# Performance work log

Hardware: AMD Instinct MI355X
Metric: run time of the kernel (lower is better)

## Reference

```python
import jax, jax.numpy as jnp
import numpy as np

D_MODEL = 1024
H = 16
D_K = D_MODEL // H
D_FF = 4096
EPS = 1e-6


def setup_inputs() -> dict:
    key = jax.random.key(0)
    ks = jax.random.split(key, 16)
    s = 1.0 / np.sqrt(D_MODEL)
    sf = 1.0 / np.sqrt(D_FF)
    inp = {
        'x': jax.random.normal(ks[0], (4, 2048, D_MODEL), dtype=jnp.float32),
        'wq': jax.random.uniform(ks[1], (D_MODEL, D_MODEL), minval=-s, maxval=s),
        'bq': jax.random.uniform(ks[2], (D_MODEL,), minval=-s, maxval=s),
        'wk': jax.random.uniform(ks[3], (D_MODEL, D_MODEL), minval=-s, maxval=s),
        'bk': jax.random.uniform(ks[4], (D_MODEL,), minval=-s, maxval=s),
        'wv': jax.random.uniform(ks[5], (D_MODEL, D_MODEL), minval=-s, maxval=s),
        'bv': jax.random.uniform(ks[6], (D_MODEL,), minval=-s, maxval=s),
        'wo': jax.random.uniform(ks[7], (D_MODEL, D_MODEL), minval=-s, maxval=s),
        'bo': jax.random.uniform(ks[8], (D_MODEL,), minval=-s, maxval=s),
        'w1': jax.random.uniform(ks[9], (D_MODEL, D_FF), minval=-s, maxval=s),
        'b1': jax.random.uniform(ks[10], (D_FF,), minval=-s, maxval=s),
        'w2': jax.random.uniform(ks[11], (D_FF, D_MODEL), minval=-sf, maxval=sf),
        'b2': jax.random.uniform(ks[12], (D_MODEL,), minval=-sf, maxval=sf),
        'alpha1': jnp.ones((1,), jnp.float32),
        'bias1': jnp.zeros((1,), jnp.float32),
        'alpha2': jnp.ones((1,), jnp.float32),
        'bias2': jnp.zeros((1,), jnp.float32),
    }
    return inp


def _layer_norm(x, alpha, bias):
    # torch: alpha*(x-mean)/(std+eps)+bias with unbiased std (ddof=1), eps on std
    m = jnp.mean(x, axis=-1, keepdims=True)
    s = jnp.std(x, axis=-1, keepdims=True, ddof=1)
    return alpha * (x - m) / (s + EPS) + bias


def _mha(x, wq, bq, wk, bk, wv, bv, wo, bo):
    B, S, _ = x.shape
    q = (x @ wq + bq).reshape(B, S, H, D_K).transpose(0, 2, 1, 3)
    k = (x @ wk + bk).reshape(B, S, H, D_K).transpose(0, 2, 1, 3)
    v = (x @ wv + bv).reshape(B, S, H, D_K).transpose(0, 2, 1, 3)
    scores = jnp.einsum('bhqd,bhkd->bhqk', q, k) / np.sqrt(D_K)
    attn = jax.nn.softmax(scores, axis=-1)
    out = jnp.einsum('bhqk,bhkd->bhqd', attn, v)
    out = out.transpose(0, 2, 1, 3).reshape(B, S, D_MODEL)
    return out @ wo + bo


def reference(x, wq, bq, wk, bk, wv, bv, wo, bo, w1, b1, w2, b2,
              alpha1, bias1, alpha2, bias2):
    # Residual 1: x + MHA(LN(x))
    h = x + _mha(_layer_norm(x, alpha1, bias1), wq, bq, wk, bk, wv, bv, wo, bo)
    # Residual 2: h + FFN(LN(h)); FFN = W2 relu(W1 z + b1) + b2
    z = _layer_norm(h, alpha2, bias2)
    ffn = jax.nn.relu(z @ w1 + b1) @ w2 + b2
    return h + ffn
```

## Files before the change

### kernel.cpp

```cpp
#include <hip/hip_runtime.h>
#include <hip/hip_bf16.h>
#include <cstdint>
#include <cstddef>

typedef __bf16 bf16;
typedef __bf16 bf16x4 __attribute__((ext_vector_type(4)));
typedef __bf16 bf16x8 __attribute__((ext_vector_type(8)));
typedef float f32x4 __attribute__((ext_vector_type(4)));

#define QK_SCALE 0.1803368801111204f

#define AS1 __attribute__((address_space(1)))
#define AS3 __attribute__((address_space(3)))

__device__ __forceinline__ void gload_lds16(const void* g, void* l) {
  __builtin_amdgcn_global_load_lds((AS1 void*)g, (AS3 void*)l, 16, 0, 0);
}

__device__ __forceinline__ float b2f(unsigned short u) {
  union { unsigned int i; float f; } v; v.i = (unsigned int)u << 16; return v.f;
}

__global__ __launch_bounds__(256)
void transpose_cvt(const float* __restrict__ in, bf16* __restrict__ out,
                   int K, int N) {
  __shared__ float t[32][33];
  const int tx = threadIdx.x, ty = threadIdx.y;
  const int n0 = blockIdx.x * 32, k0 = blockIdx.y * 32;
#pragma unroll
  for (int j = ty; j < 32; j += 8)
    t[j][tx] = in[(size_t)(k0 + j) * N + n0 + tx];
  __syncthreads();
#pragma unroll
  for (int j = ty; j < 32; j += 8)
    out[(size_t)(n0 + j) * K + k0 + tx] = (bf16)t[tx][j];
}

__global__ __launch_bounds__(256)
void transpose_cvt4(const float* __restrict__ wq, const float* __restrict__ wk,
                    const float* __restrict__ wv, const float* __restrict__ wo,
                    bf16* __restrict__ wqkvT, bf16* __restrict__ woT) {
  __shared__ float t[32][33];
  const int tx = threadIdx.x, ty = threadIdx.y, z = blockIdx.z;
  const float* in = (z == 0) ? wq : (z == 1) ? wk : (z == 2) ? wv : wo;
  bf16* out = (z < 3) ? wqkvT + (size_t)z * 1024 * 1024 : woT;
  const float sc = (z == 0) ? QK_SCALE : 1.0f;
  const int n0 = blockIdx.x * 32, k0 = blockIdx.y * 32;
#pragma unroll
  for (int j = ty; j < 32; j += 8)
    t[j][tx] = in[(size_t)(k0 + j) * 1024 + n0 + tx] * sc;
  __syncthreads();
#pragma unroll
  for (int j = ty; j < 32; j += 8)
    out[(size_t)(n0 + j) * 1024 + k0 + tx] = (bf16)t[tx][j];
}

__global__ __launch_bounds__(256)
void concat_bias(const float* __restrict__ bq, const float* __restrict__ bk,
                 const float* __restrict__ bv, float* __restrict__ o) {
  int i = blockIdx.x * 256 + threadIdx.x;
  if (i < 1024) o[i] = bq[i] * QK_SCALE;
  else if (i < 2048) o[i] = bk[i - 1024];
  else o[i] = bv[i - 2048];
}

__global__ __launch_bounds__(256)
void ln_kernel(const float* __restrict__ x, bf16* __restrict__ y,
               const float* __restrict__ alpha_p, const float* __restrict__ beta_p) {
  const int row = blockIdx.x;
  const float4 v = ((const float4*)(x + (size_t)row * 1024))[threadIdx.x];
  float s = v.x + v.y + v.z + v.w;
  float ss = v.x * v.x + v.y * v.y + v.z * v.z + v.w * v.w;
#pragma unroll
  for (int m = 1; m < 64; m <<= 1) {
    s += __shfl_xor(s, m);
    ss += __shfl_xor(ss, m);
  }
  __shared__ float red[8];
  const int wave = threadIdx.x >> 6, lane = threadIdx.x & 63;
  if (lane == 0) { red[wave] = s; red[4 + wave] = ss; }
  __syncthreads();
  s = red[0] + red[1] + red[2] + red[3];
  ss = red[4] + red[5] + red[6] + red[7];
  const float mean = s * (1.0f / 1024.0f);
  const float var = fmaxf(ss - 1024.0f * mean * mean, 0.0f) * (1.0f / 1023.0f);
  const float k = alpha_p[0] / (sqrtf(var) + 1e-6f);
  const float beta = beta_p[0];
  union { bf16 b[4]; uint2 u; } pk;
  pk.b[0] = (bf16)((v.x - mean) * k + beta);
  pk.b[1] = (bf16)((v.y - mean) * k + beta);
  pk.b[2] = (bf16)((v.z - mean) * k + beta);
  pk.b[3] = (bf16)((v.w - mean) * k + beta);
  ((uint2*)(y + (size_t)row * 1024))[threadIdx.x] = pk.u;
}

template <typename OutT, bool RELU, bool RESID>
__global__ __launch_bounds__(256)
void gemm_bt(const bf16* __restrict__ A, const bf16* __restrict__ Bt,
             const float* __restrict__ bias, const float* __restrict__ resid,
             OutT* __restrict__ C, int M, int N, int K) {
  __shared__ __align__(16) bf16 As[2][128 * 32];
  __shared__ __align__(16) bf16 Bs[2][128 * 32];
  const int tid = threadIdx.x;
  const int wave = tid >> 6, lane = tid & 63;
  const int l16 = lane & 15, lq = lane >> 4;
  const int nwg = gridDim.x * gridDim.y;
  const int id = blockIdx.y * gridDim.x + blockIdx.x;
  const int w = (id & 7) * (nwg >> 3) + (id >> 3);
  const int bm = (w / gridDim.y) * 128, bn = (w % gridDim.y) * 128;
  const int wr = wave >> 1, wc = wave & 1;

  const int tmp = (lane * 16) ^ (((lane >> 3) & 7) << 4);
  const int srow = tmp >> 6, sseg = (tmp >> 4) & 3;
  const bf16* Ab = A + (size_t)bm * K + sseg * 8;
  const bf16* Bb = Bt + (size_t)bn * K + sseg * 8;

  auto STAGE = [&](int k0, int buf) {
#pragma unroll
    for (int i = 0; i < 2; i++) {
      const int chunk = wave * 2 + i;
      const int r = chunk * 16 + srow;
      gload_lds16(Ab + (size_t)r * K + k0, (char*)As[buf] + chunk * 1024);
      gload_lds16(Bb + (size_t)r * K + k0, (char*)Bs[buf] + chunk * 1024);
    }
  };
  auto swz = [&](int row) -> int {
    return (row >> 1) * 128 + (((((row & 1) << 2) | lq) ^ ((row >> 1) & 7)) << 4);
  };

  STAGE(0, 0);
  __syncthreads();

  f32x4 acc[4][4] = {};
  const int nk = K >> 5;
  for (int t = 0; t < nk; t++) {
    const int cur = t & 1;
    if (t + 1 < nk) STAGE((t + 1) << 5, cur ^ 1);
    bf16x8 a[4], b[4];
#pragma unroll
    for (int m = 0; m < 4; m++)
      a[m] = *(const bf16x8*)((const char*)As[cur] + swz(wr * 64 + m * 16 + l16));
#pragma unroll
    for (int n = 0; n < 4; n++)
      b[n] = *(const bf16x8*)((const char*)Bs[cur] + swz(wc * 64 + n * 16 + l16));
#pragma unroll
    for (int m = 0; m < 4; m++)
#pragma unroll
      for (int n = 0; n < 4; n++)
        acc[m][n] = __builtin_amdgcn_mfma_f32_16x16x32_bf16(a[m], b[n], acc[m][n], 0, 0, 0);
    __syncthreads();
  }
#pragma unroll
  for (int m = 0; m < 4; m++) {
    const int row0 = bm + wr * 64 + m * 16 + lq * 4;
#pragma unroll
    for (int n = 0; n < 4; n++) {
      const int col = bn + wc * 64 + n * 16 + l16;
      const float bv = bias[col];
#pragma unroll
      for (int j = 0; j < 4; j++) {
        float v = acc[m][n][j] + bv;
        if (RELU) v = fmaxf(v, 0.0f);
        if (RESID) v += resid[(size_t)(row0 + j) * N + col];
        C[(size_t)(row0 + j) * N + col] = (OutT)v;
      }
    }
  }
}

template <typename OutT, bool RELU, bool BIAS>
__global__ __launch_bounds__(512, 2)
void gemm_v4(const bf16* __restrict__ A, const bf16* __restrict__ Bt,
             const float* __restrict__ bias, OutT* __restrict__ C,
             int lda, int ldb, int ldc, int K,
             int azs, int bzs, size_t czs) {
  __shared__ __align__(16) char lds[4 * 32768];
  const int tid = threadIdx.x;
  const int wave = tid >> 6, lane = tid & 63;
  const int l16 = lane & 15, lq = lane >> 4;
  const int wr = wave >> 2, wc = wave & 3;
  const int nwg = gridDim.x * gridDim.y;
  const int id = blockIdx.y * gridDim.x + blockIdx.x;
  const int w = (id & 7) * (nwg >> 3) + (id >> 3);
  const int bm = (w / gridDim.y) * 256, bn = (w % gridDim.y) * 256;

  A  += (size_t)blockIdx.z * azs;
  Bt += (size_t)blockIdx.z * bzs;
  C  += (size_t)blockIdx.z * czs;

  const int p = lane >> 3, jj = (lane & 7) ^ p;
  const int lrow = p * 2 + (jj >> 2), lseg = jj & 3;
  const bf16* Abase = A + (size_t)bm * lda + lseg * 8;
  const bf16* Bbase = Bt + (size_t)bn * ldb + lseg * 8;

  auto STAGEH = [&](int t, int half) {
    const int k0 = t << 5;
    const int grow = (half & 1) * 128 + wave * 16 + lrow;
    const void* src = (half < 2) ? (const void*)(Abase + (size_t)grow * lda + k0)
                                 : (const void*)(Bbase + (size_t)grow * ldb + k0);
    gload_lds16(src, lds + (t & 3) * 32768 + (half >> 1) * 16384 +
                         (half & 1) * 8192 + wave * 1024);
  };
  auto swz = [&](int row) -> int {
    return (row >> 1) * 128 + (((((row & 1) << 2) | lq) ^ ((row >> 1) & 7)) << 4);
  };

  const int nkt = K >> 5;
#pragma unroll
  for (int hh = 0; hh < 4; hh++) STAGEH(0, hh);
#pragma unroll
  for (int hh = 0; hh < 4; hh++) STAGEH(1, hh);
  asm volatile("s_waitcnt vmcnt(4)" ::: "memory");
  __builtin_amdgcn_s_barrier();

  f32x4 acc[8][4] = {};
  for (int t = 0; t < nkt; t++) {
    const char* bufA = lds + (t & 3) * 32768;
    const char* bufB = bufA + 16384;
    bf16x8 a0[4], b0[4], a1[4];
#pragma unroll
    for (int i = 0; i < 4; i++)
      a0[i] = *(const bf16x8*)(bufA + swz(wr * 128 + i * 16 + l16));
#pragma unroll
    for (int n = 0; n < 4; n++)
      b0[n] = *(const bf16x8*)(bufB + swz(wc * 64 + n * 16 + l16));
    if (t + 2 < nkt) { STAGEH(t + 2, 0); STAGEH(t + 2, 2); }
    __builtin_amdgcn_s_barrier();
    asm volatile("s_waitcnt lgkmcnt(0)" ::: "memory");
    __builtin_amdgcn_sched_barrier(0);
    __builtin_amdgcn_s_setprio(1);
#pragma unroll
    for (int i = 0; i < 4; i++)
#pragma unroll
      for (int n = 0; n < 4; n++)
        acc[i][n] = __builtin_amdgcn_mfma_f32_16x16x32_bf16(a0[i], b0[n], acc[i][n], 0, 0, 0);
    __builtin_amdgcn_s_setprio(0);
    __builtin_amdgcn_s_barrier();
#pragma unroll
    for (int i = 0; i < 4; i++)
      a1[i] = *(const bf16x8*)(bufA + swz(wr * 128 + 64 + i * 16 + l16));
    if (t + 2 < nkt) { STAGEH(t + 2, 1); STAGEH(t + 2, 3); }
    if (t + 2 < nkt) asm volatile("s_waitcnt vmcnt(4)" ::: "memory");
    else             asm volatile("s_waitcnt vmcnt(0)" ::: "memory");
    __builtin_amdgcn_s_barrier();
    asm volatile("s_waitcnt lgkmcnt(0)" ::: "memory");
    __builtin_amdgcn_sched_barrier(0);
    __builtin_amdgcn_s_setprio(1);
#pragma unroll
    for (int i = 0; i < 4; i++)
#pragma unroll
      for (int n = 0; n < 4; n++)
        acc[4 + i][n] = __builtin_amdgcn_mfma_f32_16x16x32_bf16(a1[i], b0[n], acc[4 + i][n], 0, 0, 0);
    __builtin_amdgcn_s_setprio(0);
    __builtin_amdgcn_s_barrier();
  }
#pragma unroll
  for (int m = 0; m < 8; m++) {
    const int row0 = bm + wr * 128 + m * 16 + lq * 4;
#pragma unroll
    for (int n = 0; n < 4; n++) {
      const int col = bn + wc * 64 + n * 16 + l16;
      const float bv = BIAS ? bias[col] : 0.0f;
#pragma unroll
      for (int j = 0; j < 4; j++) {
        float v = acc[m][n][j] + bv;
        if (RELU) v = fmaxf(v, 0.0f);
        C[(size_t)(row0 + j) * ldc + col] = (OutT)v;
      }
    }
  }
}

__global__ __launch_bounds__(256)
void ffn2_reduce(const bf16* __restrict__ p0, const bf16* __restrict__ p1,
                 const float* __restrict__ b2, float* __restrict__ out) {
  const size_t i = (size_t)blockIdx.x * 256 + threadIdx.x;
  float4 h = ((const float4*)out)[i];
  const ushort4 a = ((const ushort4*)p0)[i];
  const ushort4 b = ((const ushort4*)p1)[i];
  const float4 bb = ((const float4*)b2)[i & 255];
  h.x += b2f(a.x) + b2f(b.x) + bb.x;
  h.y += b2f(a.y) + b2f(b.y) + bb.y;
  h.z += b2f(a.z) + b2f(b.z) + bb.z;
  h.w += b2f(a.w) + b2f(b.w) + bb.w;
  ((float4*)out)[i] = h;
}

__global__ __launch_bounds__(256)
void vt_prep(const bf16* __restrict__ qkv, bf16* __restrict__ Vt) {
  __shared__ __align__(16) bf16 Vl[64 * 64];
  const int tid = threadIdx.x;
  const int sblk = blockIdx.x, bh = blockIdx.y, b = bh >> 4, h = bh & 15;
  const size_t srow = (size_t)b * 2048 + sblk * 64;
  const bf16* src = qkv + srow * 3072 + 2048 + h * 64;
#pragma unroll
  for (int i = 0; i < 2; i++) {
    int c = i * 256 + tid;
    int s = c >> 3, dseg = c & 7;
    int col = dseg ^ (s & 7) ^ (s >> 3);
    *(uint4*)((char*)Vl + s * 128 + col * 16) =
        *(const uint4*)(src + (size_t)s * 3072 + dseg * 8);
  }
  __syncthreads();
  bf16* dst = Vt + (size_t)bh * 64 * 2048 + sblk * 64;
#pragma unroll
  for (int i = 0; i < 2; i++) {
    int c = i * 256 + tid;
    int d = c >> 3, grp = c & 7;
    union { bf16 v[8]; uint4 u; } pk;
#pragma unroll
    for (int j = 0; j < 8; j++) {
      int pp = grp * 8 + j;
      int s = (pp & 32) | (((pp >> 2) & 1) << 4) | (((pp >> 3) & 3) << 2) | (pp & 3);
      int col = (d >> 3) ^ (s & 7) ^ (s >> 3);
      pk.v[j] = *(const bf16*)((char*)Vl + s * 128 + col * 16 + ((2 * d) & 15));
    }
    *(uint4*)(dst + (size_t)d * 2048 + grp * 8) = pk.u;
  }
}

__global__ __launch_bounds__(256, 2)
void attn_kernel(const bf16* __restrict__ qkv, const bf16* __restrict__ Vt,
                 bf16* __restrict__ out) {
  __shared__ __align__(16) bf16 smem[40960];
  bf16* Qs = smem;
  bf16* Ks = smem + 16384;
  bf16* Vs = smem + 28672;
  const int tid = threadIdx.x, wave = tid >> 6, lane = tid & 63;
  const int l16 = lane & 15, lq = lane >> 4;
  const int id = blockIdx.y * 8 + blockIdx.x;
  const int w = (id & 7) * 64 + (id >> 3);
  const int qblk = w & 7, bh = w >> 3;
  const int b = bh >> 4, h = bh & 15;
  const int q0 = qblk * 256;
  const size_t rowbase = (size_t)b * 2048;
  const bf16* Qg = qkv + (rowbase + q0) * 3072 + h * 64;
  const bf16* Kg = qkv + rowbase * 3072 + 1024 + h * 64;
  const bf16* Vg = Vt + (size_t)bh * 64 * 2048;

#pragma unroll
  for (int i = 0; i < 8; i++) {
    const int c = i * 256 + wave * 64;
    const int cl = c + lane;
    const int r = cl >> 3, seg = cl & 7;
    gload_lds16(Qg + (size_t)r * 3072 + (seg ^ (r & 7)) * 8, (char*)Qs + c * 16);
  }
  auto stageKV = [&](int kt, int buf) {
    const int kv0 = kt * 64;
#pragma unroll
    for (int i = 0; i < 2; i++) {
      const int c = i * 256 + wave * 64;
      const int cl = c + lane;
      const int r = cl >> 3, seg = cl & 7;
      gload_lds16(Kg + (size_t)(kv0 + r) * 3072 + (seg ^ (r & 7)) * 8,
                  (char*)Ks + buf * 8192 + c * 16);
      gload_lds16(Vg + (size_t)r * 2048 + kv0 + (seg ^ (r & 7)) * 8,
                  (char*)Vs + buf * 8192 + c * 16);
    }
  };
  stageKV(0, 0);
  stageKV(1, 1);

  asm volatile("s_waitcnt vmcnt(8)" ::: "memory");
  __builtin_amdgcn_s_barrier();
  bf16x8 qb[4][2];
#pragma unroll
  for (int g = 0; g < 4; g++)
#pragma unroll
    for (int H = 0; H < 2; H++) {
      const int row = wave * 64 + g * 16 + l16;
      const int col = (H * 64 + lq * 16) ^ ((row & 7) << 4);
      qb[g][H] = *(const bf16x8*)((const char*)Qs + row * 128 + col);
    }

  f32x4 oacc[4][4] = {};
  f32x4 lacc[4] = {};
  bf16x8 onesb;
#pragma unroll
  for (int j = 0; j < 8; j++) onesb[j] = (bf16)1.0f;

  for (int t = 0; t < 32; t++) {
    if (t < 31) asm volatile("s_waitcnt vmcnt(4)" ::: "memory");
    else        asm volatile("s_waitcnt vmcnt(0)" ::: "memory");
    __builtin_amdgcn_s_barrier();
    __builtin_amdgcn_sched_barrier(0);
    if (t + 2 < 32) stageKV(t + 2, (t + 2) % 3);
    const char* Kb = (const char*)Ks + (t % 3) * 8192;
    const char* Vb = (const char*)Vs + (t % 3) * 8192;

    bf16x8 ka[2][4];
#pragma unroll
    for (int H = 0; H < 2; H++)
#pragma unroll
      for (int m = 0; m < 4; m++) {
        const int row = m * 16 + l16;
        const int col = (H * 64 + lq * 16) ^ ((row & 7) << 4);
        ka[H][m] = *(const bf16x8*)(Kb + row * 128 + col);
      }
    bf16x8 vb[2][4];
#pragma unroll
    for (int H = 0; H < 2; H++)
#pragma unroll
      for (int nd = 0; nd < 4; nd++) {
        const int row = nd * 16 + l16;
        const int col = (H * 64 + lq * 16) ^ ((row & 7) << 4);
        vb[H][nd] = *(const bf16x8*)(Vb + row * 128 + col);
      }
#pragma unroll
    for (int g = 0; g < 4; g++) {
      f32x4 sc[4];
      __builtin_amdgcn_s_setprio(1);
#pragma unroll
      for (int m = 0; m < 4; m++) {
        f32x4 z = {};
        sc[m] = __builtin_amdgcn_mfma_f32_16x16x32_bf16(ka[0][m], qb[g][0], z, 0, 0, 0);
        sc[m] = __builtin_amdgcn_mfma_f32_16x16x32_bf16(ka[1][m], qb[g][1], sc[m], 0, 0, 0);
      }
      __builtin_amdgcn_s_setprio(0);
      bf16x8 pa0, pa1;
#pragma unroll
      for (int m = 0; m < 2; m++)
#pragma unroll
        for (int r = 0; r < 4; r++)
          pa0[m * 4 + r] = (bf16)__builtin_amdgcn_exp2f(sc[m][r]);
#pragma unroll
      for (int m = 0; m < 2; m++)
#pragma unroll
        for (int r = 0; r < 4; r++)
          pa1[m * 4 + r] = (bf16)__builtin_amdgcn_exp2f(sc[2 + m][r]);
      __builtin_amdgcn_s_setprio(1);
#pragma unroll
      for (int nd = 0; nd < 4; nd++) {
        oacc[g][nd] = __builtin_amdgcn_mfma_f32_16x16x32_bf16(pa0, vb[0][nd], oacc[g][nd], 0, 0, 0);
        oacc[g][nd] = __builtin_amdgcn_mfma_f32_16x16x32_bf16(pa1, vb[1][nd], oacc[g][nd], 0, 0, 0);
      }
      lacc[g] = __builtin_amdgcn_mfma_f32_16x16x32_bf16(pa0, onesb, lacc[g], 0, 0, 0);
      lacc[g] = __builtin_amdgcn_mfma_f32_16x16x32_bf16(pa1, onesb, lacc[g], 0, 0, 0);
      __builtin_amdgcn_s_setprio(0);
    }
  }
#pragma unroll
  for (int g = 0; g < 4; g++) {
#pragma unroll
    for (int r = 0; r < 4; r++) {
      const float inv = 1.0f / lacc[g][r];
      const size_t row = rowbase + q0 + wave * 64 + g * 16 + lq * 4 + r;
#pragma unroll
      for (int nd = 0; nd < 4; nd++)
        out[row * 1024 + h * 64 + nd * 16 + l16] = (bf16)(oacc[g][nd][r] * inv);
    }
  }
}

extern "C" void kernel_launch(void* const* d_in, const int* in_sizes, int n_in,
                              void* d_out, int out_size, void* d_ws, size_t ws_size,
                              hipStream_t stream) {
  const float* x      = (const float*)d_in[0];
  const float* wq     = (const float*)d_in[1];
  const float* bq     = (const float*)d_in[2];
  const float* wk     = (const float*)d_in[3];
  const float* bk     = (const float*)d_in[4];
  const float* wv     = (const float*)d_in[5];
  const float* bv     = (const float*)d_in[6];
  const float* wo     = (const float*)d_in[7];
  const float* bo     = (const float*)d_in[8];
  const float* w1     = (const float*)d_in[9];
  const float* b1     = (const float*)d_in[10];
  const float* w2     = (const float*)d_in[11];
  const float* b2     = (const float*)d_in[12];
  const float* alpha1 = (const float*)d_in[13];
  const float* bias1  = (const float*)d_in[14];
  const float* alpha2 = (const float*)d_in[15];
  const float* bias2  = (const float*)d_in[16];
  float* out = (float*)d_out;

  const size_t MB = 1024ull * 1024ull;
  char* ws = (char*)d_ws;
  bf16*  wqkvT = (bf16*)(ws);
  bf16*  woT   = (bf16*)(ws + 6 * MB);
  bf16*  w1T   = (bf16*)(ws + 8 * MB);
  bf16*  w2T   = (bf16*)(ws + 16 * MB);
  float* bqkv  = (float*)(ws + 24 * MB);
  bf16*  Z     = (bf16*)(ws + 24 * MB + 65536);
  bf16*  Vtb   = Z;
  bf16*  QKV   = (bf16*)(ws + 40 * MB + 65536);
  bf16*  AO    = (bf16*)(ws + 88 * MB + 65536);
  bf16*  FFN1  = QKV;
  bf16*  PART  = (bf16*)ws;
  const size_t PART1_OFF = (24 * MB + 65536) / 2;

  const dim3 tb(32, 8);
  transpose_cvt4<<<dim3(32, 32, 4), tb, 0, stream>>>(wq, wk, wv, wo, wqkvT, woT);
  transpose_cvt<<<dim3(128, 32), tb, 0, stream>>>(w1, w1T, 1024, 4096);
  transpose_cvt<<<dim3(32, 128), tb, 0, stream>>>(w2, w2T, 4096, 1024);
  concat_bias<<<12, 256, 0, stream>>>(bq, bk, bv, bqkv);

  ln_kernel<<<8192, 256, 0, stream>>>(x, Z, alpha1, bias1);
  gemm_v4<bf16, false, true><<<dim3(32, 12), 512, 0, stream>>>(
      Z, wqkvT, bqkv, QKV, 1024, 1024, 3072, 1024, 0, 0, 0);
  vt_prep<<<dim3(32, 64), 256, 0, stream>>>(QKV, Vtb);
  attn_kernel<<<dim3(8, 64), 256, 0, stream>>>(QKV, Vtb, AO);
  gemm_bt<float, false, true><<<dim3(64, 8), 256, 0, stream>>>(
      AO, woT, bo, x, out, 8192, 1024, 1024);
  ln_kernel<<<8192, 256, 0, stream>>>(out, Z, alpha2, bias2);
  gemm_v4<bf16, true, true><<<dim3(32, 16), 512, 0, stream>>>(
      Z, w1T, b1, FFN1, 1024, 1024, 4096, 1024, 0, 0, 0);
  gemm_v4<bf16, false, false><<<dim3(32, 4, 2), 512, 0, stream>>>(
      FFN1, w2T, nullptr, PART, 4096, 4096, 1024, 2048, 2048, 2048, PART1_OFF);
  ffn2_reduce<<<8192, 256, 0, stream>>>(PART, PART + PART1_OFF, b2, out);
}
```

Measured before the change: 354.8 us.

## Replace 256x256 GEMM with 256x128 BK=64 triple-buffered kernel, fuse split-K reduce

Replaces the 256x256-tile, K=32, four-buffer GEMM with a 256x128 tile using K=64 steps and three LDS buffers, with a new row-XOR swizzle and 8 waves each computing 64x64. The FFN2 split-K now runs as two sequential launches: the second half writes a bf16 partial, and the first half adds that partial, the bias and the residual in its epilogue, which removes the separate reduce kernel. The smaller tiles double the grid size to improve CU occupancy and tail balance, at the cost of more operand re-reads per output and serialising the two split-K halves.

```diff
diff --git a/kernel.cpp b/kernel.cpp
--- a/kernel.cpp
+++ b/kernel.cpp
@@ -97,8 +97,8 @@
 template <typename OutT, bool RELU, bool RESID>
 __global__ __launch_bounds__(256)
 void gemm_bt(const bf16* __restrict__ A, const bf16* __restrict__ Bt,
-             const float* __restrict__ bias, const float* __restrict__ resid,
-             OutT* __restrict__ C, int M, int N, int K) {
+             const float* __restrict__ bias, const float* resid,
+             OutT* C, int M, int N, int K) {
   __shared__ __align__(16) bf16 As[2][128 * 32];
   __shared__ __align__(16) bf16 Bs[2][128 * 32];
   const int tid = threadIdx.x;
@@ -168,122 +168,114 @@
   }
 }
 
-template <typename OutT, bool RELU, bool BIAS>
+template <typename OutT, bool RELU, bool BIAS, bool RESID, bool ADDP>
 __global__ __launch_bounds__(512, 2)
-void gemm_v4(const bf16* __restrict__ A, const bf16* __restrict__ Bt,
-             const float* __restrict__ bias, OutT* __restrict__ C,
-             int lda, int ldb, int ldc, int K,
-             int azs, int bzs, size_t czs) {
-  __shared__ __align__(16) char lds[4 * 32768];
+void gemm_v6(const bf16* __restrict__ A, const bf16* __restrict__ Bt,
+             const float* __restrict__ bias, const float* resid,
+             const bf16* __restrict__ padd, OutT* C,
+             int lda, int ldb, int ldc, int K) {
+  __shared__ __align__(16) char lds[3 * 49152];
   const int tid = threadIdx.x;
   const int wave = tid >> 6, lane = tid & 63;
   const int l16 = lane & 15, lq = lane >> 4;
-  const int wr = wave >> 2, wc = wave & 3;
+  const int wm = wave >> 1, wn = wave & 1;
   const int nwg = gridDim.x * gridDim.y;
   const int id = blockIdx.y * gridDim.x + blockIdx.x;
   const int w = (id & 7) * (nwg >> 3) + (id >> 3);
-  const int bm = (w / gridDim.y) * 256, bn = (w % gridDim.y) * 256;
-
-  A  += (size_t)blockIdx.z * azs;
-  Bt += (size_t)blockIdx.z * bzs;
-  C  += (size_t)blockIdx.z * czs;
-
-  const int p = lane >> 3, jj = (lane & 7) ^ p;
-  const int lrow = p * 2 + (jj >> 2), lseg = jj & 3;
-  const bf16* Abase = A + (size_t)bm * lda + lseg * 8;
-  const bf16* Bbase = Bt + (size_t)bn * ldb + lseg * 8;
-
-  auto STAGEH = [&](int t, int half) {
-    const int k0 = t << 5;
-    const int grow = (half & 1) * 128 + wave * 16 + lrow;
-    const void* src = (half < 2) ? (const void*)(Abase + (size_t)grow * lda + k0)
-                                 : (const void*)(Bbase + (size_t)grow * ldb + k0);
-    gload_lds16(src, lds + (t & 3) * 32768 + (half >> 1) * 16384 +
-                         (half & 1) * 8192 + wave * 1024);
+  const int bm = (w / gridDim.y) * 256, bn = (w % gridDim.y) * 128;
+
+  const bf16* Abase = A + (size_t)bm * lda;
+  const bf16* Bbase = Bt + (size_t)bn * ldb;
+  const int r8 = tid >> 3, seg = tid & 7;
+
+  auto STAGEP = [&](int t, int p) {
+    const int k0 = t << 6;
+    char* dst = lds + (t % 3) * 49152;
+#pragma unroll
+    for (int i = 0; i < 2; i++) {
+      const int ii = p * 2 + i;
+      const int r = ii * 64 + r8;
+      gload_lds16(Abase + (size_t)r * lda + k0 + (seg ^ (r & 7)) * 8,
+                  dst + ii * 8192 + tid * 16);
+    }
+    const int rb = p * 64 + r8;
+    gload_lds16(Bbase + (size_t)rb * ldb + k0 + (seg ^ (rb & 7)) * 8,
+                dst + 32768 + p * 8192 + tid * 16);
   };
-  auto swz = [&](int row) -> int {
-    return (row >> 1) * 128 + (((((row & 1) << 2) | lq) ^ ((row >> 1) & 7)) << 4);
+  auto fo = [&](int row, int kh) -> int {
+    return row * 128 + ((((kh << 2) | lq) ^ (row & 7)) << 4);
   };
 
-  const int nkt = K >> 5;
-#pragma unroll
-  for (int hh = 0; hh < 4; hh++) STAGEH(0, hh);
-#pragma unroll
-  for (int hh = 0; hh < 4; hh++) STAGEH(1, hh);
-  asm volatile("s_waitcnt vmcnt(4)" ::: "memory");
+  const int nkt = K >> 6;
+  STAGEP(0, 0); STAGEP(0, 1);
+  STAGEP(1, 0); STAGEP(1, 1);
+  asm volatile("s_waitcnt vmcnt(6)" ::: "memory");
   __builtin_amdgcn_s_barrier();
 
-  f32x4 acc[8][4] = {};
+  f32x4 acc[4][4] = {};
   for (int t = 0; t < nkt; t++) {
-    const char* bufA = lds + (t & 3) * 32768;
-    const char* bufB = bufA + 16384;
-    bf16x8 a0[4], b0[4], a1[4];
-#pragma unroll
-    for (int i = 0; i < 4; i++)
-      a0[i] = *(const bf16x8*)(bufA + swz(wr * 128 + i * 16 + l16));
-#pragma unroll
-    for (int n = 0; n < 4; n++)
-      b0[n] = *(const bf16x8*)(bufB + swz(wc * 64 + n * 16 + l16));
-    if (t + 2 < nkt) { STAGEH(t + 2, 0); STAGEH(t + 2, 2); }
+    const char* buf = lds + (t % 3) * 49152;
+    bf16x8 a[4], b[4];
+#pragma unroll
+    for (int mf = 0; mf < 4; mf++)
+      a[mf] = *(const bf16x8*)(buf + fo(wm * 64 + mf * 16 + l16, 0));
+#pragma unroll
+    for (int nf = 0; nf < 4; nf++)
+      b[nf] = *(const bf16x8*)(buf + 32768 + fo(wn * 64 + nf * 16 + l16, 0));
+    if (t + 2 < nkt) STAGEP(t + 2, 0);
     __builtin_amdgcn_s_barrier();
     asm volatile("s_waitcnt lgkmcnt(0)" ::: "memory");
     __builtin_amdgcn_sched_barrier(0);
     __builtin_amdgcn_s_setprio(1);
 #pragma unroll
-    for (int i = 0; i < 4; i++)
-#pragma unroll
-      for (int n = 0; n < 4; n++)
-        acc[i][n] = __builtin_amdgcn_mfma_f32_16x16x32_bf16(a0[i], b0[n], acc[i][n], 0, 0, 0);
+    for (int mf = 0; mf < 4; mf++)
+#pragma unroll
+      for (int nf = 0; nf < 4; nf++)
+        acc[mf][nf] = __builtin_amdgcn_mfma_f32_16x16x32_bf16(a[mf], b[nf], acc[mf][nf], 0, 0, 0);
     __builtin_amdgcn_s_setprio(0);
     __builtin_amdgcn_s_barrier();
 #pragma unroll
-    for (int i = 0; i < 4; i++)
-      a1[i] = *(const bf16x8*)(bufA + swz(wr * 128 + 64 + i * 16 + l16));
-    if (t + 2 < nkt) { STAGEH(t + 2, 1); STAGEH(t + 2, 3); }
-    if (t + 2 < nkt) asm volatile("s_waitcnt vmcnt(4)" ::: "memory");
-    else             asm volatile("s_waitcnt vmcnt(0)" ::: "memory");
+    for (int mf = 0; mf < 4; mf++)
+      a[mf] = *(const bf16x8*)(buf + fo(wm * 64 + mf * 16 + l16, 1));
+#pragma unroll
+    for (int nf = 0; nf < 4; nf++)
+      b[nf] = *(const bf16x8*)(buf + 32768 + fo(wn * 64 + nf * 16 + l16, 1));
+    if (t + 2 < nkt) {
+      STAGEP(t + 2, 1);
+      asm volatile("s_waitcnt vmcnt(6)" ::: "memory");
+    } else {
+      asm volatile("s_waitcnt vmcnt(0)" ::: "memory");
+    }
     __builtin_amdgcn_s_barrier();
     asm volatile("s_waitcnt lgkmcnt(0)" ::: "memory");
     __builtin_amdgcn_sched_barrier(0);
     __builtin_amdgcn_s_setprio(1);
 #pragma unroll
-    for (int i = 0; i < 4; i++)
-#pragma unroll
-      for (int n = 0; n < 4; n++)
-        acc[4 + i][n] = __builtin_amdgcn_mfma_f32_16x16x32_bf16(a1[i], b0[n], acc[4 + i][n], 0, 0, 0);
+    for (int mf = 0; mf < 4; mf++)
+#pragma unroll
+      for (int nf = 0; nf < 4; nf++)
+        acc[mf][nf] = __builtin_amdgcn_mfma_f32_16x16x32_bf16(a[mf], b[nf], acc[mf][nf], 0, 0, 0);
     __builtin_amdgcn_s_setprio(0);
     __builtin_amdgcn_s_barrier();
   }
 #pragma unroll
-  for (int m = 0; m < 8; m++) {
-    const int row0 = bm + wr * 128 + m * 16 + lq * 4;
-#pragma unroll
-    for (int n = 0; n < 4; n++) {
-      const int col = bn + wc * 64 + n * 16 + l16;
+  for (int mf = 0; mf < 4; mf++) {
+    const int row0 = bm + wm * 64 + mf * 16 + lq * 4;
+#pragma unroll
+    for (int nf = 0; nf < 4; nf++) {
+      const int col = bn + wn * 64 + nf * 16 + l16;
       const float bv = BIAS ? bias[col] : 0.0f;
 #pragma unroll
       for (int j = 0; j < 4; j++) {
-        float v = acc[m][n][j] + bv;
+        const size_t idx = (size_t)(row0 + j) * ldc + col;
+        float v = acc[mf][nf][j] + bv;
         if (RELU) v = fmaxf(v, 0.0f);
-        C[(size_t)(row0 + j) * ldc + col] = (OutT)v;
+        if (ADDP) v += b2f(((const unsigned short*)padd)[idx]);
+        if (RESID) v += resid[idx];
+        C[idx] = (OutT)v;
       }
     }
   }
-}
-
-__global__ __launch_bounds__(256)
-void ffn2_reduce(const bf16* __restrict__ p0, const bf16* __restrict__ p1,
-                 const float* __restrict__ b2, float* __restrict__ out) {
-  const size_t i = (size_t)blockIdx.x * 256 + threadIdx.x;
-  float4 h = ((const float4*)out)[i];
-  const ushort4 a = ((const ushort4*)p0)[i];
-  const ushort4 b = ((const ushort4*)p1)[i];
-  const float4 bb = ((const float4*)b2)[i & 255];
-  h.x += b2f(a.x) + b2f(b.x) + bb.x;
-  h.y += b2f(a.y) + b2f(b.y) + bb.y;
-  h.z += b2f(a.z) + b2f(b.z) + bb.z;
-  h.w += b2f(a.w) + b2f(b.w) + bb.w;
-  ((float4*)out)[i] = h;
 }
 
 __global__ __launch_bounds__(256)
@@ -486,8 +478,7 @@
   bf16*  QKV   = (bf16*)(ws + 40 * MB + 65536);
   bf16*  AO    = (bf16*)(ws + 88 * MB + 65536);
   bf16*  FFN1  = QKV;
-  bf16*  PART  = (bf16*)ws;
-  const size_t PART1_OFF = (24 * MB + 65536) / 2;
+  bf16*  PART1 = Z;
 
   const dim3 tb(32, 8);
   transpose_cvt4<<<dim3(32, 32, 4), tb, 0, stream>>>(wq, wk, wv, wo, wqkvT, woT);
@@ -496,16 +487,18 @@
   concat_bias<<<12, 256, 0, stream>>>(bq, bk, bv, bqkv);
 
   ln_kernel<<<8192, 256, 0, stream>>>(x, Z, alpha1, bias1);
-  gemm_v4<bf16, false, true><<<dim3(32, 12), 512, 0, stream>>>(
-      Z, wqkvT, bqkv, QKV, 1024, 1024, 3072, 1024, 0, 0, 0);
+  gemm_v6<bf16, false, true, false, false><<<dim3(32, 24), 512, 0, stream>>>(
+      Z, wqkvT, bqkv, nullptr, nullptr, QKV, 1024, 1024, 3072, 1024);
   vt_prep<<<dim3(32, 64), 256, 0, stream>>>(QKV, Vtb);
   attn_kernel<<<dim3(8, 64), 256, 0, stream>>>(QKV, Vtb, AO);
   gemm_bt<float, false, true><<<dim3(64, 8), 256, 0, stream>>>(
       AO, woT, bo, x, out, 8192, 1024, 1024);
   ln_kernel<<<8192, 256, 0, stream>>>(out, Z, alpha2, bias2);
-  gemm_v4<bf16, true, true><<<dim3(32, 16), 512, 0, stream>>>(
-      Z, w1T, b1, FFN1, 1024, 1024, 4096, 1024, 0, 0, 0);
-  gemm_v4<bf16, false, false><<<dim3(32, 4, 2), 512, 0, stream>>>(
-      FFN1, w2T, nullptr, PART, 4096, 4096, 1024, 2048, 2048, 2048, PART1_OFF);
-  ffn2_reduce<<<8192, 256, 0, stream>>>(PART, PART + PART1_OFF, b2, out);
-}
+  gemm_v6<bf16, true, true, false, false><<<dim3(32, 32), 512, 0, stream>>>(
+      Z, w1T, b1, nullptr, nullptr, FFN1, 1024, 1024, 4096, 1024);
+  gemm_v6<bf16, false, false, false, false><<<dim3(32, 8), 512, 0, stream>>>(
+      FFN1 + 2048, w2T + 2048, nullptr, nullptr, nullptr, PART1,
+      4096, 4096, 1024, 2048);
+  gemm_v6<float, false, true, true, true><<<dim3(32, 8), 512, 0, stream>>>(
+      FFN1, w2T, b2, out, PART1, out, 4096, 4096, 1024, 2048);
+}
```

Result: slower. 380.0 us (+7.1%).
